# Optimization experiments

Measured on AMD Instinct MI355X. Metric: run time of the kernel, lower is better.

Reference implementation:

```python
import jax, jax.numpy as jnp
import numpy as np
from math import sqrt

B, N, D = 8, 4096, 512

def rotary(x, phases):
    # x: [B,N,D], phases: [B,N,D/2]
    c, s = jnp.cos(phases), jnp.sin(phases)
    a, b = jnp.split(x, 2, axis=-1)
    return jnp.concatenate([a * c - b * s, a * s + b * c], axis=-1)

def setup_inputs() -> dict:
    key = jax.random.key(0)
    ks = jax.random.split(key, 8)
    phi = jax.random.normal(ks[0], (B, N, D), dtype=jnp.float32)
    coords = jax.random.normal(ks[1], (B, N, 3), dtype=jnp.float32)
    weights = jax.random.uniform(ks[2], (B, N), dtype=jnp.float32)
    std = 1.0 / sqrt(D)
    Wq = jax.random.normal(ks[3], (D, D), dtype=jnp.float32) * std
    Wk = jax.random.normal(ks[4], (D, D), dtype=jnp.float32) * std
    Wv = jax.random.normal(ks[5], (D, D), dtype=jnp.float32) * std
    bq = jnp.zeros((D,), jnp.float32)
    bk = jnp.zeros((D,), jnp.float32)
    bv = jnp.zeros((D,), jnp.float32)
    # mode_lift weight, std = 1/kernel_scale with kernel_scale=1.0
    Wrot = jax.random.normal(ks[6], (D // 2, 3), dtype=jnp.float32)
    return {"phi": phi, "coords": coords, "weights": weights,
            "Wq": Wq, "bq": bq, "Wk": Wk, "bk": bk, "Wv": Wv, "bv": bv,
            "Wrot": Wrot}

def reference(phi, coords, weights, Wq, bq, Wk, bk, Wv, bv, Wrot):
    d = phi.shape[-1]
    q = phi @ Wq.T + bq
    k = phi @ Wk.T + bk
    v = phi @ Wv.T + bv
    # _normalize: scale query by 1/sqrt(d); attach quadrature weights to value
    q = q * (1.0 / sqrt(d))
    v = weights[..., None] * v
    # rotary positional encoding on q and k
    phases = jnp.einsum('bnc,dc->bnd', coords, Wrot)  # [B,N,D/2]
    q = rotary(q, phases)
    k = rotary(k, phases)
    # linear attention: q @ (k^T @ v), O(N*d^2)
    kv = jnp.einsum('bnd,bne->bde', k, v)   # [B,D,D]
    return jnp.einsum('bnd,bde->bne', q, kv)  # [B,N,D]
```

## Files before the change

kernel.cpp:

```cpp
#include <hip/hip_runtime.h>


typedef _Float16 f16x8 __attribute__((ext_vector_type(8)));
typedef _Float16 f16x4 __attribute__((ext_vector_type(4)));
typedef float f32x4 __attribute__((ext_vector_type(4)));

__device__ __forceinline__ void gl_lds16(const void* g, void* l) {
    __builtin_amdgcn_global_load_lds(
        (const __attribute__((address_space(1))) void*)g,
        (__attribute__((address_space(3))) void*)l, 16, 0, 0);
}

__device__ __forceinline__ void stage2(const _Float16* gA, size_t sA,
                                       const _Float16* gB, size_t sB,
                                       _Float16* As, _Float16* Bs,
                                       int ca, int srow, int sseg) {
    gl_lds16(&gA[(size_t)(ca * 16 + srow) * sA + sseg], &As[ca * 512]);
    gl_lds16(&gA[(size_t)(ca * 16 + 16 + srow) * sA + sseg], &As[(ca + 1) * 512]);
    gl_lds16(&gB[(size_t)(ca * 16 + srow) * sB + sseg], &Bs[ca * 512]);
    gl_lds16(&gB[(size_t)(ca * 16 + 16 + srow) * sB + sseg], &Bs[(ca + 1) * 512]);
}

__device__ __forceinline__ void mfma_step(const _Float16* As, const _Float16* Bs,
                                          int wm, int wn, int l16, int quad,
                                          f32x4 acc[4][4]) {
    f16x8 af[4], bf[4];
    #pragma unroll
    for (int mi = 0; mi < 4; mi++)
        af[mi] = *(const f16x8*)&As[(wm + mi * 16 + l16) * 32 + quad * 8];
    #pragma unroll
    for (int ni = 0; ni < 4; ni++)
        bf[ni] = *(const f16x8*)&Bs[(wn + ni * 16 + l16) * 32 + quad * 8];
    #pragma unroll
    for (int mi = 0; mi < 4; mi++)
        #pragma unroll
        for (int ni = 0; ni < 4; ni++)
            acc[mi][ni] = __builtin_amdgcn_mfma_f32_16x16x32_f16(
                af[mi], bf[ni], acc[mi][ni], 0, 0, 0);
}

__global__ __launch_bounds__(256) void convert_phi(const float* __restrict__ phi,
                                                   _Float16* __restrict__ phi_h) {
    int i = (blockIdx.x * 256 + threadIdx.x) * 4;
    float4 v = *(const float4*)(phi + i);
    f16x4 o = {(_Float16)v.x, (_Float16)v.y, (_Float16)v.z, (_Float16)v.w};
    *(f16x4*)(phi_h + i) = o;
}

__global__ __launch_bounds__(256) void pack_w(
    const float* __restrict__ Wq, const float* __restrict__ Wk,
    const float* __restrict__ Wv, const float* __restrict__ bq,
    const float* __restrict__ bk, const float* __restrict__ bv,
    _Float16* __restrict__ wcat, float* __restrict__ bcat) {
    int j = blockIdx.x;
    int reg = j >> 9, jr = j & 511;
    const float* W; const float* bias;
    if (reg == 0)      { W = Wq; bias = bq; }
    else if (reg == 1) { W = Wk; bias = bk; }
    else               { W = Wv; bias = bv; }
    int d = (reg < 2) ? ((jr & 1) ? (jr >> 1) + 256 : (jr >> 1)) : jr;
    for (int i = threadIdx.x; i < 512; i += 256)
        wcat[j * 512 + i] = (_Float16)W[d * 512 + i];
    if (threadIdx.x == 0) bcat[j] = bias[d];
}

__global__ __launch_bounds__(256) void qkv_kernel(
    const _Float16* __restrict__ phi_h, const _Float16* __restrict__ wcat,
    const float* __restrict__ bcat, const float* __restrict__ coords,
    const float* __restrict__ weights, const float* __restrict__ Wrot,
    _Float16* __restrict__ qr, _Float16* __restrict__ krT,
    _Float16* __restrict__ vwT) {
    __shared__ __align__(16) char smem[34816];
    _Float16* As0 = (_Float16*)smem;
    _Float16* Bs0 = (_Float16*)(smem + 8192);
    _Float16* As1 = (_Float16*)(smem + 16384);
    _Float16* Bs1 = (_Float16*)(smem + 24576);
    _Float16* Ts  = (_Float16*)smem;

    const int tid = threadIdx.x;
    const int lane = tid & 63, wave = tid >> 6;
    const int quad = lane >> 4, l16 = lane & 15;
    const int wm = (wave >> 1) * 64, wn = (wave & 1) * 64;
    const int m0 = blockIdx.y * 128;
    const int c0 = blockIdx.x * 128;
    const int ca = wave * 2;
    const int srow = lane >> 2, sseg = (lane & 3) * 8;

    const _Float16* gA = phi_h + (size_t)m0 * 512;
    const _Float16* gB = wcat + (size_t)c0 * 512;

    f32x4 acc[4][4] = {};

    stage2(gA, 512, gB, 512, As0, Bs0, ca, srow, sseg);
    __syncthreads();
    for (int k0 = 0; k0 < 512; k0 += 64) {
        stage2(gA + k0 + 32, 512, gB + k0 + 32, 512, As1, Bs1, ca, srow, sseg);
        mfma_step(As0, Bs0, wm, wn, l16, quad, acc);
        __syncthreads();
        if (k0 + 64 < 512)
            stage2(gA + k0 + 64, 512, gB + k0 + 64, 512, As0, Bs0, ca, srow, sseg);
        mfma_step(As1, Bs1, wm, wn, l16, quad, acc);
        __syncthreads();
    }

    const int region = c0 >> 9;
    const float qscale = 0.04419417382415922f;

    float bias[4], w0[4], w1[4], w2[4];
    #pragma unroll
    for (int ni = 0; ni < 4; ni++) {
        int gc = c0 + wn + ni * 16 + l16;
        bias[ni] = bcat[gc];
        if (region < 2) {
            int jp = (gc & 511) >> 1;
            w0[ni] = Wrot[jp * 3];
            w1[ni] = Wrot[jp * 3 + 1];
            w2[ni] = Wrot[jp * 3 + 2];
        }
    }

    if (region == 0) {
        #pragma unroll
        for (int mi = 0; mi < 4; mi++)
            #pragma unroll
            for (int r = 0; r < 4; r++) {
                int row = wm + mi * 16 + quad * 4 + r;
                int gm = m0 + row;
                float x = coords[gm * 3], y = coords[gm * 3 + 1], z = coords[gm * 3 + 2];
                #pragma unroll
                for (int ni = 0; ni < 4; ni++) {
                    float val = (acc[mi][ni][r] + bias[ni]) * qscale;
                    float part = __shfl_xor(val, 1);
                    float ph = x * w0[ni] + y * w1[ni] + z * w2[ni];
                    float sv, cv; __sincosf(ph, &sv, &cv);
                    float res = (l16 & 1) ? (part * sv + val * cv)
                                          : (val * cv - part * sv);
                    Ts[row * 136 + wn + ni * 16 + l16] = (_Float16)res;
                }
            }
        __syncthreads();
        for (int i = tid; i < 2048; i += 256) {
            int row = i >> 4, cv = (i & 15) * 8;
            *(f16x8*)&qr[(m0 + row) * 512 + c0 + cv] = *(f16x8*)&Ts[row * 136 + cv];
        }
    } else {
        #pragma unroll
        for (int mi = 0; mi < 4; mi++)
            #pragma unroll
            for (int r = 0; r < 4; r++) {
                int row = wm + mi * 16 + quad * 4 + r;
                int gm = m0 + row;
                if (region == 1) {
                    float x = coords[gm * 3], y = coords[gm * 3 + 1], z = coords[gm * 3 + 2];
                    #pragma unroll
                    for (int ni = 0; ni < 4; ni++) {
                        float val = acc[mi][ni][r] + bias[ni];
                        float part = __shfl_xor(val, 1);
                        float ph = x * w0[ni] + y * w1[ni] + z * w2[ni];
                        float sv, cv; __sincosf(ph, &sv, &cv);
                        float res = (l16 & 1) ? (part * sv + val * cv)
                                              : (val * cv - part * sv);
                        Ts[(wn + ni * 16 + l16) * 136 + row] = (_Float16)res;
                    }
                } else {
                    float wgt = weights[gm];
                    #pragma unroll
                    for (int ni = 0; ni < 4; ni++) {
                        float val = (acc[mi][ni][r] + bias[ni]) * wgt;
                        Ts[(wn + ni * 16 + l16) * 136 + row] = (_Float16)val;
                    }
                }
            }
        __syncthreads();
        _Float16* dst = (region == 1) ? krT : vwT;
        const int b = m0 >> 12, n0 = m0 & 4095, cb = c0 & 511;
        for (int i = tid; i < 2048; i += 256) {
            int col = i >> 4, rv = (i & 15) * 8;
            *(f16x8*)&dst[((size_t)b * 512 + cb + col) * 4096 + n0 + rv] =
                *(f16x8*)&Ts[col * 136 + rv];
        }
    }
}

__global__ __launch_bounds__(256) void kv_kernel(
    const _Float16* __restrict__ vwT, const _Float16* __restrict__ krT,
    _Float16* __restrict__ kvp) {
    __shared__ __align__(16) char smem[32768];
    _Float16* As0 = (_Float16*)smem;
    _Float16* Bs0 = (_Float16*)(smem + 8192);
    _Float16* As1 = (_Float16*)(smem + 16384);
    _Float16* Bs1 = (_Float16*)(smem + 24576);
    const int tid = threadIdx.x, lane = tid & 63, wave = tid >> 6;
    const int quad = lane >> 4, l16 = lane & 15;
    const int wm = (wave >> 1) * 64, wn = (wave & 1) * 64;
    const int d0 = blockIdx.x * 128, e0 = blockIdx.y * 128;
    const int b = blockIdx.z >> 3, split = blockIdx.z & 7;
    const int ca = wave * 2;
    const int srow = lane >> 2, sseg = (lane & 3) * 8;
    const size_t base = (size_t)b * 512 * 4096;
    const int kbeg = split * 512;
    const _Float16* gA = vwT + base + (size_t)e0 * 4096 + kbeg;
    const _Float16* gB = krT + base + (size_t)d0 * 4096 + kbeg;
    f32x4 acc[4][4] = {};

    stage2(gA, 4096, gB, 4096, As0, Bs0, ca, srow, sseg);
    __syncthreads();
    for (int k0 = 0; k0 < 512; k0 += 64) {
        stage2(gA + k0 + 32, 4096, gB + k0 + 32, 4096, As1, Bs1, ca, srow, sseg);
        mfma_step(As0, Bs0, wm, wn, l16, quad, acc);
        __syncthreads();
        if (k0 + 64 < 512)
            stage2(gA + k0 + 64, 4096, gB + k0 + 64, 4096, As0, Bs0, ca, srow, sseg);
        mfma_step(As1, Bs1, wm, wn, l16, quad, acc);
        __syncthreads();
    }

    _Float16* dst = kvp + ((size_t)split * 8 + b) * 262144;
    #pragma unroll
    for (int mi = 0; mi < 4; mi++)
        #pragma unroll
        for (int ni = 0; ni < 4; ni++)
            #pragma unroll
            for (int r = 0; r < 4; r++) {
                int e = e0 + wm + mi * 16 + quad * 4 + r;
                int d = d0 + wn + ni * 16 + l16;
                dst[e * 512 + d] = (_Float16)acc[mi][ni][r];
            }
}

__global__ __launch_bounds__(256) void reduce_kv(const _Float16* __restrict__ kvp,
                                                 _Float16* __restrict__ kvT) {
    int i = (blockIdx.x * 256 + threadIdx.x) * 8;
    float s[8] = {};
    #pragma unroll
    for (int sp = 0; sp < 8; sp++) {
        f16x8 v = *(const f16x8*)(kvp + (size_t)sp * 2097152 + i);
        #pragma unroll
        for (int j = 0; j < 8; j++) s[j] += (float)v[j];
    }
    f16x8 o;
    #pragma unroll
    for (int j = 0; j < 8; j++) o[j] = (_Float16)s[j];
    *(f16x8*)(kvT + i) = o;
}

__global__ __launch_bounds__(256) void out_kernel(
    const _Float16* __restrict__ qr, const _Float16* __restrict__ kvT,
    float* __restrict__ out) {
    __shared__ __align__(16) char smem[32768];
    _Float16* As0 = (_Float16*)smem;
    _Float16* Bs0 = (_Float16*)(smem + 8192);
    _Float16* As1 = (_Float16*)(smem + 16384);
    _Float16* Bs1 = (_Float16*)(smem + 24576);
    const int tid = threadIdx.x, lane = tid & 63, wave = tid >> 6;
    const int quad = lane >> 4, l16 = lane & 15;
    const int wm = (wave >> 1) * 64, wn = (wave & 1) * 64;
    const int m0 = blockIdx.y * 128, e0 = blockIdx.x * 128;
    const int b = m0 >> 12;
    const int ca = wave * 2;
    const int srow = lane >> 2, sseg = (lane & 3) * 8;
    const _Float16* gA = qr + (size_t)m0 * 512;
    const _Float16* gB = kvT + (size_t)b * 262144 + (size_t)e0 * 512;
    f32x4 acc[4][4] = {};

    stage2(gA, 512, gB, 512, As0, Bs0, ca, srow, sseg);
    __syncthreads();
    for (int k0 = 0; k0 < 512; k0 += 64) {
        stage2(gA + k0 + 32, 512, gB + k0 + 32, 512, As1, Bs1, ca, srow, sseg);
        mfma_step(As0, Bs0, wm, wn, l16, quad, acc);
        __syncthreads();
        if (k0 + 64 < 512)
            stage2(gA + k0 + 64, 512, gB + k0 + 64, 512, As0, Bs0, ca, srow, sseg);
        mfma_step(As1, Bs1, wm, wn, l16, quad, acc);
        __syncthreads();
    }

    #pragma unroll
    for (int mi = 0; mi < 4; mi++)
        #pragma unroll
        for (int ni = 0; ni < 4; ni++)
            #pragma unroll
            for (int r = 0; r < 4; r++) {
                int gm = m0 + wm + mi * 16 + quad * 4 + r;
                int e = e0 + wn + ni * 16 + l16;
                out[(size_t)gm * 512 + e] = acc[mi][ni][r];
            }
}

extern "C" void kernel_launch(void* const* d_in, const int* in_sizes, int n_in,
                              void* d_out, int out_size, void* d_ws, size_t ws_size,
                              hipStream_t stream) {
    const float* phi     = (const float*)d_in[0];
    const float* coords  = (const float*)d_in[1];
    const float* weights = (const float*)d_in[2];
    const float* Wq      = (const float*)d_in[3];
    const float* bq      = (const float*)d_in[4];
    const float* Wk      = (const float*)d_in[5];
    const float* bk      = (const float*)d_in[6];
    const float* Wv      = (const float*)d_in[7];
    const float* bv      = (const float*)d_in[8];
    const float* Wrot    = (const float*)d_in[9];
    float* out = (float*)d_out;

    char* ws = (char*)d_ws;
    _Float16* phi_h = (_Float16*)(ws);
    _Float16* kvp   = (_Float16*)(ws);
    _Float16* wcat  = (_Float16*)(ws + 33554432);
    float*    bcat  = (float*)   (ws + 35127296);
    _Float16* qr    = (_Float16*)(ws + 35133440);
    _Float16* krT   = (_Float16*)(ws + 68687872);
    _Float16* vwT   = (_Float16*)(ws + 102242304);
    _Float16* kvT   = (_Float16*)(ws + 135796736);

    convert_phi<<<16384, 256, 0, stream>>>(phi, phi_h);
    pack_w<<<1536, 256, 0, stream>>>(Wq, Wk, Wv, bq, bk, bv, wcat, bcat);
    qkv_kernel<<<dim3(12, 256), 256, 0, stream>>>(phi_h, wcat, bcat, coords,
                                                  weights, Wrot, qr, krT, vwT);
    kv_kernel<<<dim3(4, 4, 64), 256, 0, stream>>>(vwT, krT, kvp);
    reduce_kv<<<1024, 256, 0, stream>>>(kvp, kvT);
    out_kernel<<<dim3(4, 256), 256, 0, stream>>>(qr, kvT, out);
}
```

Before: 319.7 us.

## Load GEMM fragments directly from global memory into registers, dropping LDS staging

```diff
diff --git a/kernel.cpp b/kernel.cpp
--- a/kernel.cpp
+++ b/kernel.cpp
@@ -5,38 +5,51 @@
 typedef _Float16 f16x4 __attribute__((ext_vector_type(4)));
 typedef float f32x4 __attribute__((ext_vector_type(4)));
 
-__device__ __forceinline__ void gl_lds16(const void* g, void* l) {
-    __builtin_amdgcn_global_load_lds(
-        (const __attribute__((address_space(1))) void*)g,
-        (__attribute__((address_space(3))) void*)l, 16, 0, 0);
-}
-
-__device__ __forceinline__ void stage2(const _Float16* gA, size_t sA,
-                                       const _Float16* gB, size_t sB,
-                                       _Float16* As, _Float16* Bs,
-                                       int ca, int srow, int sseg) {
-    gl_lds16(&gA[(size_t)(ca * 16 + srow) * sA + sseg], &As[ca * 512]);
-    gl_lds16(&gA[(size_t)(ca * 16 + 16 + srow) * sA + sseg], &As[(ca + 1) * 512]);
-    gl_lds16(&gB[(size_t)(ca * 16 + srow) * sB + sseg], &Bs[ca * 512]);
-    gl_lds16(&gB[(size_t)(ca * 16 + 16 + srow) * sB + sseg], &Bs[(ca + 1) * 512]);
-}
-
-__device__ __forceinline__ void mfma_step(const _Float16* As, const _Float16* Bs,
-                                          int wm, int wn, int l16, int quad,
-                                          f32x4 acc[4][4]) {
-    f16x8 af[4], bf[4];
+__device__ __forceinline__ void reg_gemm512(const _Float16* __restrict__ A, int lda,
+                                            const _Float16* __restrict__ B, int ldb,
+                                            int wm, int wn, int l16, int quad,
+                                            f32x4 acc[4][4]) {
+    const _Float16* pa[4];
+    const _Float16* pb[4];
     #pragma unroll
     for (int mi = 0; mi < 4; mi++)
-        af[mi] = *(const f16x8*)&As[(wm + mi * 16 + l16) * 32 + quad * 8];
+        pa[mi] = A + (size_t)(wm + mi * 16 + l16) * lda + quad * 8;
     #pragma unroll
     for (int ni = 0; ni < 4; ni++)
-        bf[ni] = *(const f16x8*)&Bs[(wn + ni * 16 + l16) * 32 + quad * 8];
-    #pragma unroll
-    for (int mi = 0; mi < 4; mi++)
-        #pragma unroll
-        for (int ni = 0; ni < 4; ni++)
-            acc[mi][ni] = __builtin_amdgcn_mfma_f32_16x16x32_f16(
-                af[mi], bf[ni], acc[mi][ni], 0, 0, 0);
+        pb[ni] = B + (size_t)(wn + ni * 16 + l16) * ldb + quad * 8;
+
+    f16x8 a0[4], b0[4], a1[4], b1[4];
+    #pragma unroll
+    for (int i = 0; i < 4; i++) {
+        a0[i] = *(const f16x8*)(pa[i]);
+        b0[i] = *(const f16x8*)(pb[i]);
+    }
+    for (int k = 0; k < 512; k += 64) {
+        #pragma unroll
+        for (int i = 0; i < 4; i++) {
+            a1[i] = *(const f16x8*)(pa[i] + k + 32);
+            b1[i] = *(const f16x8*)(pb[i] + k + 32);
+        }
+        #pragma unroll
+        for (int mi = 0; mi < 4; mi++)
+            #pragma unroll
+            for (int ni = 0; ni < 4; ni++)
+                acc[mi][ni] = __builtin_amdgcn_mfma_f32_16x16x32_f16(
+                    a0[mi], b0[ni], acc[mi][ni], 0, 0, 0);
+        if (k + 64 < 512) {
+            #pragma unroll
+            for (int i = 0; i < 4; i++) {
+                a0[i] = *(const f16x8*)(pa[i] + k + 64);
+                b0[i] = *(const f16x8*)(pb[i] + k + 64);
+            }
+        }
+        #pragma unroll
+        for (int mi = 0; mi < 4; mi++)
+            #pragma unroll
+            for (int ni = 0; ni < 4; ni++)
+                acc[mi][ni] = __builtin_amdgcn_mfma_f32_16x16x32_f16(
+                    a1[mi], b1[ni], acc[mi][ni], 0, 0, 0);
+    }
 }
 
 __global__ __launch_bounds__(256) void convert_phi(const float* __restrict__ phi,
@@ -70,12 +83,7 @@
     const float* __restrict__ weights, const float* __restrict__ Wrot,
     _Float16* __restrict__ qr, _Float16* __restrict__ krT,
     _Float16* __restrict__ vwT) {
-    __shared__ __align__(16) char smem[34816];
-    _Float16* As0 = (_Float16*)smem;
-    _Float16* Bs0 = (_Float16*)(smem + 8192);
-    _Float16* As1 = (_Float16*)(smem + 16384);
-    _Float16* Bs1 = (_Float16*)(smem + 24576);
-    _Float16* Ts  = (_Float16*)smem;
+    __shared__ __align__(16) _Float16 Ts[128 * 136];
 
     const int tid = threadIdx.x;
     const int lane = tid & 63, wave = tid >> 6;
@@ -83,25 +91,10 @@
     const int wm = (wave >> 1) * 64, wn = (wave & 1) * 64;
     const int m0 = blockIdx.y * 128;
     const int c0 = blockIdx.x * 128;
-    const int ca = wave * 2;
-    const int srow = lane >> 2, sseg = (lane & 3) * 8;
-
-    const _Float16* gA = phi_h + (size_t)m0 * 512;
-    const _Float16* gB = wcat + (size_t)c0 * 512;
 
     f32x4 acc[4][4] = {};
-
-    stage2(gA, 512, gB, 512, As0, Bs0, ca, srow, sseg);
-    __syncthreads();
-    for (int k0 = 0; k0 < 512; k0 += 64) {
-        stage2(gA + k0 + 32, 512, gB + k0 + 32, 512, As1, Bs1, ca, srow, sseg);
-        mfma_step(As0, Bs0, wm, wn, l16, quad, acc);
-        __syncthreads();
-        if (k0 + 64 < 512)
-            stage2(gA + k0 + 64, 512, gB + k0 + 64, 512, As0, Bs0, ca, srow, sseg);
-        mfma_step(As1, Bs1, wm, wn, l16, quad, acc);
-        __syncthreads();
-    }
+    reg_gemm512(phi_h + (size_t)m0 * 512, 512, wcat + (size_t)c0 * 512, 512,
+                wm, wn, l16, quad, acc);
 
     const int region = c0 >> 9;
     const float qscale = 0.04419417382415922f;
@@ -185,35 +178,18 @@
 __global__ __launch_bounds__(256) void kv_kernel(
     const _Float16* __restrict__ vwT, const _Float16* __restrict__ krT,
     _Float16* __restrict__ kvp) {
-    __shared__ __align__(16) char smem[32768];
-    _Float16* As0 = (_Float16*)smem;
-    _Float16* Bs0 = (_Float16*)(smem + 8192);
-    _Float16* As1 = (_Float16*)(smem + 16384);
-    _Float16* Bs1 = (_Float16*)(smem + 24576);
     const int tid = threadIdx.x, lane = tid & 63, wave = tid >> 6;
     const int quad = lane >> 4, l16 = lane & 15;
     const int wm = (wave >> 1) * 64, wn = (wave & 1) * 64;
     const int d0 = blockIdx.x * 128, e0 = blockIdx.y * 128;
     const int b = blockIdx.z >> 3, split = blockIdx.z & 7;
-    const int ca = wave * 2;
-    const int srow = lane >> 2, sseg = (lane & 3) * 8;
     const size_t base = (size_t)b * 512 * 4096;
     const int kbeg = split * 512;
-    const _Float16* gA = vwT + base + (size_t)e0 * 4096 + kbeg;
-    const _Float16* gB = krT + base + (size_t)d0 * 4096 + kbeg;
+
     f32x4 acc[4][4] = {};
-
-    stage2(gA, 4096, gB, 4096, As0, Bs0, ca, srow, sseg);
-    __syncthreads();
-    for (int k0 = 0; k0 < 512; k0 += 64) {
-        stage2(gA + k0 + 32, 4096, gB + k0 + 32, 4096, As1, Bs1, ca, srow, sseg);
-        mfma_step(As0, Bs0, wm, wn, l16, quad, acc);
-        __syncthreads();
-        if (k0 + 64 < 512)
-            stage2(gA + k0 + 64, 4096, gB + k0 + 64, 4096, As0, Bs0, ca, srow, sseg);
-        mfma_step(As1, Bs1, wm, wn, l16, quad, acc);
-        __syncthreads();
-    }
+    reg_gemm512(vwT + base + (size_t)e0 * 4096 + kbeg, 4096,
+                krT + base + (size_t)d0 * 4096 + kbeg, 4096,
+                wm, wn, l16, quad, acc);
 
     _Float16* dst = kvp + ((size_t)split * 8 + b) * 262144;
     #pragma unroll
@@ -247,33 +223,16 @@
 __global__ __launch_bounds__(256) void out_kernel(
     const _Float16* __restrict__ qr, const _Float16* __restrict__ kvT,
     float* __restrict__ out) {
-    __shared__ __align__(16) char smem[32768];
-    _Float16* As0 = (_Float16*)smem;
-    _Float16* Bs0 = (_Float16*)(smem + 8192);
-    _Float16* As1 = (_Float16*)(smem + 16384);
-    _Float16* Bs1 = (_Float16*)(smem + 24576);
     const int tid = threadIdx.x, lane = tid & 63, wave = tid >> 6;
     const int quad = lane >> 4, l16 = lane & 15;
     const int wm = (wave >> 1) * 64, wn = (wave & 1) * 64;
     const int m0 = blockIdx.y * 128, e0 = blockIdx.x * 128;
     const int b = m0 >> 12;
-    const int ca = wave * 2;
-    const int srow = lane >> 2, sseg = (lane & 3) * 8;
-    const _Float16* gA = qr + (size_t)m0 * 512;
-    const _Float16* gB = kvT + (size_t)b * 262144 + (size_t)e0 * 512;
+
     f32x4 acc[4][4] = {};
-
-    stage2(gA, 512, gB, 512, As0, Bs0, ca, srow, sseg);
-    __syncthreads();
-    for (int k0 = 0; k0 < 512; k0 += 64) {
-        stage2(gA + k0 + 32, 512, gB + k0 + 32, 512, As1, Bs1, ca, srow, sseg);
-        mfma_step(As0, Bs0, wm, wn, l16, quad, acc);
-        __syncthreads();
-        if (k0 + 64 < 512)
-            stage2(gA + k0 + 64, 512, gB + k0 + 64, 512, As0, Bs0, ca, srow, sseg);
-        mfma_step(As1, Bs1, wm, wn, l16, quad, acc);
-        __syncthreads();
-    }
+    reg_gemm512(qr + (size_t)m0 * 512, 512,
+                kvT + (size_t)b * 262144 + (size_t)e0 * 512, 512,
+                wm, wn, l16, quad, acc);
 
     #pragma unroll
     for (int mi = 0; mi < 4; mi++)
```

After: 471.8 us. 1.48x slower.
